# Performance work log

Measured on AMD Instinct MI355X. Metric: run time of the kernel, lower is better.

## Reference

```python
import jax, jax.numpy as jnp
import numpy as np

H_DIM = 256
N_HEADS = 8
HALF = H_DIM // 2

def _lin(x, W, b):
    # torch nn.Linear: y = x @ W.T + b
    y = x @ W.T
    return y + b if b is not None else y

def setup_inputs() -> dict:
    key = jax.random.key(0)
    ks = jax.random.split(key, 16)
    s = 0.02
    d = {
        'x': jax.random.normal(ks[0], (16, H_DIM, 32, 32), jnp.float32),
        'q1_w': jax.random.normal(ks[1], (HALF, HALF), jnp.float32) * s,
        'q1_b': jnp.zeros((HALF,), jnp.float32),
        'q2_w': jax.random.normal(ks[2], (HALF, HALF), jnp.float32) * s,
        'q2_b': jnp.zeros((HALF,), jnp.float32),
        'k1_w': jax.random.normal(ks[3], (HALF, HALF), jnp.float32) * s,
        'k1_b': jnp.zeros((HALF,), jnp.float32),
        'k2_w': jax.random.normal(ks[4], (HALF, HALF), jnp.float32) * s,
        'k2_b': jnp.zeros((HALF,), jnp.float32),
        'v1_w': jax.random.normal(ks[5], (HALF, HALF), jnp.float32) * s,
        'v1_b': jnp.zeros((HALF,), jnp.float32),
        'v2_w': jax.random.normal(ks[6], (HALF, HALF), jnp.float32) * s,
        'v2_b': jnp.zeros((HALF,), jnp.float32),
        'proj1_w': jax.random.normal(ks[7], (HALF, HALF), jnp.float32) * s,
        'proj1_b': jnp.zeros((HALF,), jnp.float32),
        'proj2_w': jax.random.normal(ks[8], (HALF, HALF), jnp.float32) * s,
        'proj2_b': jnp.zeros((HALF,), jnp.float32),
        'logit_scale': jnp.log(10.0 * jnp.ones((N_HEADS, 1, 1), jnp.float32)),
        'mlp_w1': jax.random.normal(ks[9], (128, 2), jnp.float32) * s,
        'mlp_b1': jnp.zeros((128,), jnp.float32),
        'mlp_w2': jax.random.normal(ks[10], (N_HEADS, 128), jnp.float32) * s,
    }
    return d

def _rel_pos_index(h, w):
    # static (numpy) relative position index, shape [N, N]
    ch, cw = np.meshgrid(np.arange(h), np.arange(w), indexing='ij')
    coords = np.stack([ch.reshape(-1), cw.reshape(-1)])  # [2, N]
    rel = coords[:, :, None] - coords[:, None, :]         # [2, N, N]
    rel = rel.transpose(1, 2, 0)
    rel[:, :, 0] += h - 1
    rel[:, :, 1] += w - 1
    return rel[:, :, 0] * (2 * w - 1) + rel[:, :, 1]

def _forward(x, q1_w, q1_b, q2_w, q2_b, k1_w, k1_b, k2_w, k2_b,
             v1_w, v1_b, v2_w, v2_b, proj1_w, proj1_b, proj2_w, proj2_b,
             logit_scale, mlp_w1, mlp_b1, mlp_w2):
    b, c, h, w = x.shape
    N = h * w
    nh = N_HEADS
    hd = c // nh
    x3 = jnp.transpose(x, (0, 2, 3, 1)).reshape(b, N, c)
    x0, x1 = x3[..., :c // 2], x3[..., c // 2:]

    def qkv(W0, b0, W1, b1):
        t = jnp.concatenate([x0 + _lin(x0, W0, b0), x1 + _lin(x1, W1, b1)], axis=-1)
        return t.reshape(b, N, nh, hd).transpose(0, 2, 1, 3)  # [b, nh, N, hd]

    q = qkv(q1_w, q1_b, q2_w, q2_b)
    k = qkv(k1_w, k1_b, k2_w, k2_b)
    v = qkv(v1_w, v1_b, v2_w, v2_b)

    eps = 1e-12
    qn = q / jnp.maximum(jnp.linalg.norm(q, axis=-1, keepdims=True), eps)
    kn = k / jnp.maximum(jnp.linalg.norm(k, axis=-1, keepdims=True), eps)
    attn = jnp.einsum('bhnd,bhmd->bhnm', qn, kn)  # cosine similarity
    scale = jnp.exp(jnp.minimum(logit_scale, jnp.log(1.0 / 0.01)))  # [nh,1,1]
    attn = attn * scale[None]

    # continuous relative-position bias (CPB) table via small MLP
    rch = jnp.arange(-(h - 1), h, dtype=jnp.float32) / (h - 1 + 1e-8)
    rcw = jnp.arange(-(w - 1), w, dtype=jnp.float32) / (w - 1 + 1e-8)
    gh, gw = jnp.meshgrid(rch, rcw, indexing='ij')
    tab = jnp.stack([gh, gw], axis=-1) * 3.2               # [2h-1, 2w-1, 2]
    tab = jnp.sign(tab) * (1.0 - jnp.exp(-jnp.abs(tab)))
    tab = jax.nn.relu(_lin(tab, mlp_w1, mlp_b1))
    tab = _lin(tab, mlp_w2, None).reshape(-1, nh)          # [(2h-1)(2w-1), nh]

    idx = jnp.asarray(_rel_pos_index(h, w))                # [N, N]
    bias = tab[idx.reshape(-1)].reshape(N, N, nh).transpose(2, 0, 1)
    bias = 16.0 * jax.nn.sigmoid(bias)
    attn = attn + bias[None]

    attn = jax.nn.softmax(attn, axis=-1)
    out = jnp.einsum('bhnm,bhmd->bhnd', attn, v).transpose(0, 2, 1, 3).reshape(b, N, c)
    o0, o1 = out[..., :c // 2], out[..., c // 2:]
    out = jnp.concatenate([_lin(o0, proj1_w, proj1_b), _lin(o1, proj2_w, proj2_b)], axis=-1)
    return out.reshape(b, h, w, c).transpose(0, 3, 1, 2)

def reference(x, q1_w, q1_b, q2_w, q2_b, k1_w, k1_b, k2_w, k2_b,
              v1_w, v1_b, v2_w, v2_b, proj1_w, proj1_b, proj2_w, proj2_b,
              logit_scale, mlp_w1, mlp_b1, mlp_w2):
    return _forward(x, q1_w, q1_b, q2_w, q2_b, k1_w, k1_b, k2_w, k2_b,
                    v1_w, v1_b, v2_w, v2_b, proj1_w, proj1_b, proj2_w, proj2_b,
                    logit_scale, mlp_w1, mlp_b1, mlp_w2)
```

## Files before the change

kernel.cpp:

```cpp
#include <hip/hip_runtime.h>
#include <cmath>


typedef _Float16 half_t;
typedef __attribute__((ext_vector_type(2))) __fp16 fp16x2;
typedef __attribute__((ext_vector_type(4))) _Float16 half4;
typedef __attribute__((ext_vector_type(8))) _Float16 half8;
typedef __attribute__((ext_vector_type(2))) float float2v;
typedef __attribute__((ext_vector_type(4))) float float4v;
typedef __attribute__((ext_vector_type(4))) unsigned int uint4v;

static __device__ __forceinline__ float4v mfma16(half8 a, half8 b, float4v c) {
  return __builtin_amdgcn_mfma_f32_16x16x32_f16(a, b, c, 0, 0, 0);
}

struct PtrArr8 { const float* p[8]; };

__global__ __launch_bounds__(256) void prep_w(PtrArr8 wsrc, PtrArr8 bsrc,
                                              half_t* __restrict__ wf,
                                              float* __restrict__ bws) {
  int y = blockIdx.y;
  const float* src = nullptr;
  const float* bs = nullptr;
#pragma unroll
  for (int i = 0; i < 8; i++)
    if (i == y) { src = wsrc.p[i]; bs = bsrc.p[i]; }
  int flat = (blockIdx.x * 256 + threadIdx.x) * 4;
  float4 w = *(const float4*)(src + flat);
  int j = flat >> 7, k = flat & 127;
  if (y < 6) {
    if (k == j)     w.x += 1.0f;
    if (k + 1 == j) w.y += 1.0f;
    if (k + 2 == j) w.z += 1.0f;
    if (k + 3 == j) w.w += 1.0f;
  }
  half4 h;
  h[0] = (half_t)w.x;
  h[1] = (half_t)w.y;
  h[2] = (half_t)w.z;
  h[3] = (half_t)w.w;
  int ng = j >> 4, l = j & 15, ks = k >> 5, quad = (k >> 3) & 3, o8 = k & 7;
  *(half4*)(wf + y * 16384 + ((ng * 4 + ks) * 64 + quad * 16 + l) * 8 + o8) =
      h;
  if (blockIdx.x == 0 && threadIdx.x < 128)
    bws[y * 128 + threadIdx.x] = bs[threadIdx.x];
}

__global__ __launch_bounds__(256) void bias_mlp(const float* __restrict__ w1,
                                                const float* __restrict__ b1,
                                                const float* __restrict__ w2,
                                                const float* __restrict__ ls,
                                                float* __restrict__ tabh2) {
  __shared__ float sw1[256];
  __shared__ float sb1[128];
  __shared__ float sw2[1024];
  int t = threadIdx.x;
  sw1[t] = w1[t];
  if (t < 128) sb1[t] = b1[t];
  for (int i = t; i < 1024; i += 256) sw2[i] = w2[i];
  __syncthreads();
  int p = blockIdx.x * 256 + t;
  if (p >= 3969) return;
  int ph = p / 63, pw = p % 63;
  float t0 = (float)(ph - 31) * (3.2f / 31.0f);
  float t1 = (float)(pw - 31) * (3.2f / 31.0f);
  t0 = copysignf(1.0f - __expf(-fabsf(t0)), t0);
  t1 = copysignf(1.0f - __expf(-fabsf(t1)), t1);
  float acc[8];
#pragma unroll
  for (int hh = 0; hh < 8; hh++) acc[hh] = 0.0f;
  for (int j = 0; j < 128; j++) {
    float hj = fmaxf(0.0f, t0 * sw1[2 * j] + t1 * sw1[2 * j + 1] + sb1[j]);
#pragma unroll
    for (int hh = 0; hh < 8; hh++) acc[hh] += hj * sw2[hh * 128 + j];
  }
  const float L2E = 1.44269504f;
#pragma unroll
  for (int hh = 0; hh < 8; hh++) {
    float scale = __expf(fminf(ls[hh], 4.6051702f));
    float c14 = 14.0f - (scale + 16.0f) * L2E;
    float bias = 16.0f / (1.0f + __expf(-acc[hh]));
    tabh2[hh * 3969 + p] = bias * L2E + c14;
  }
}

__global__ __launch_bounds__(256, 4) void qkv_mfma(
    const float* __restrict__ x, const half_t* __restrict__ wfrag,
    const float* __restrict__ lscale, const float* __restrict__ bws,
    half_t* __restrict__ qf, half_t* __restrict__ kf,
    half_t* __restrict__ vf) {
  __shared__ half_t tbuf[4608];
  int t = threadIdx.x;
  int lane = t & 63, wv = t >> 6, l = lane & 15, quad = lane >> 4;
  int rw = wv & 1, cw = wv >> 1;
  int hf = blockIdx.y;
  int m0 = blockIdx.x * 32;
  int b = m0 >> 10, n0 = m0 & 1023;

  half8 afr[4];
  {
    const float* xb =
        x + ((size_t)b * 256 + hf * 128) * 1024 + n0 + rw * 16 + l;
#pragma unroll
    for (int ks = 0; ks < 4; ks++) {
      half8 a;
#pragma unroll
      for (int j = 0; j < 8; j++)
        a[j] = (half_t)xb[(size_t)(ks * 32 + quad * 8 + j) * 1024];
      afr[ks] = a;
    }
  }

  for (int op = 0; op < 3; op++) {
    int combo = op * 2 + hf;
    const half_t* wfb = wfrag + combo * 16384;
    float4v acc[4];
#pragma unroll
    for (int ngl = 0; ngl < 4; ngl++) {
      int ng = cw * 4 + ngl;
      float4v c = {0.f, 0.f, 0.f, 0.f};
#pragma unroll
      for (int ks = 0; ks < 4; ks++) {
        half8 bfrag =
            *(const half8*)(wfb + ((ng * 4 + ks) * 64 + lane) * 8);
        c = mfma16(afr[ks], bfrag, c);
      }
      acc[ngl] = c;
    }
#pragma unroll
    for (int ngl = 0; ngl < 4; ngl++) {
      float bb = bws[combo * 128 + (cw * 4 + ngl) * 16 + l];
#pragma unroll
      for (int r2 = 0; r2 < 4; r2++) acc[ngl][r2] += bb;
    }
    if (op < 2) {
#pragma unroll
      for (int hgl = 0; hgl < 2; hgl++) {
        float sc = 1.0f;
        if (op == 0)
          sc = __expf(fminf(lscale[hf * 4 + cw * 2 + hgl], 4.6051702f)) *
               1.44269504f;
#pragma unroll
        for (int r2 = 0; r2 < 4; r2++) {
          float ss = acc[2 * hgl][r2] * acc[2 * hgl][r2] +
                     acc[2 * hgl + 1][r2] * acc[2 * hgl + 1][r2];
          ss += __shfl_xor(ss, 1, 64);
          ss += __shfl_xor(ss, 2, 64);
          ss += __shfl_xor(ss, 4, 64);
          ss += __shfl_xor(ss, 8, 64);
          float rn = sc / fmaxf(sqrtf(ss), 1e-12f);
          acc[2 * hgl][r2] *= rn;
          acc[2 * hgl + 1][r2] *= rn;
        }
      }
#pragma unroll
      for (int ngl = 0; ngl < 4; ngl++)
#pragma unroll
        for (int r2 = 0; r2 < 4; r2++)
          tbuf[(rw * 16 + quad * 4 + r2) * 136 + (cw * 4 + ngl) * 16 + l] =
              (half_t)acc[ngl][r2];
      __syncthreads();
      half_t* dst = (op == 0) ? qf : kf;
#pragma unroll
      for (int i = 0; i < 2; i++) {
        int idx = t + 256 * i;
        int row = idx >> 4, colc = (idx & 15) * 8;
        half8 vv = *(const half8*)(tbuf + row * 136 + colc);
        int head = hf * 4 + (colc >> 5), d = colc & 31;
        *(half8*)(dst + (((size_t)b * 8 + head) * 1024 + n0 + row) * 32 + d) =
            vv;
      }
      __syncthreads();
    } else {
#pragma unroll
      for (int ngl = 0; ngl < 4; ngl++) {
        int col = (cw * 4 + ngl) * 16 + l;
        half4 hv;
#pragma unroll
        for (int r2 = 0; r2 < 4; r2++) hv[r2] = (half_t)acc[ngl][r2];
        *(half4*)(tbuf + col * 36 + rw * 16 + quad * 4) = hv;
      }
      __syncthreads();
      int p64 = (n0 >> 5) & 1;
      int nb64 = n0 & ~63;
#pragma unroll
      for (int i = 0; i < 8; i++) {
        int idx = t + 256 * i;
        int col = idx >> 4, rp = idx & 15;
        unsigned int val = *(const unsigned int*)(tbuf + col * 36 + rp * 2);
        int head = hf * 4 + (col >> 5);
        int d = col & 31;
        int npos = nb64 + ((rp >> 1) & 3) * 16 + (rp & 1) * 8 + p64 * 4 +
                   ((rp >> 3) & 1) * 2;
        *(unsigned int*)((char*)vf +
                         (((((size_t)b * 8 + head) * 32 + d) * 1024) + npos) *
                             2) = val;
      }
    }
  }
}


#define LOADK(kt)                                                           \
  {                                                                         \
    _Pragma("unroll") for (int nt = 0; nt < 4; nt++)                        \
        kfr[nt] = *(const half8*)(kbase + ((kt)*64 + nt * 16 + l) * 32 +    \
                                  quad * 8);                                \
  }

#define LOADV(kt)                                                           \
  {                                                                         \
    _Pragma("unroll") for (int ks = 0; ks < 2; ks++) {                      \
      vv0[ks] = *(const half8*)(vbase + l * 1024 + (kt)*64 + quad * 16 +    \
                                ks * 8);                                    \
      vv1[ks] = *(const half8*)(vbase + (16 + l) * 1024 + (kt)*64 +         \
                                quad * 16 + ks * 8);                        \
    }                                                                       \
  }

#define QK_PHASE(kt, S, SR)                                                 \
  {                                                                         \
    int rowb = (wv + 31 - 2 * (kt)) * 63 + cA + (S)*16;                     \
    _Pragma("unroll") for (int nt = 0; nt < 4; nt++) {                      \
      int base = rowb - (nt >> 1) * 63 - (nt & 1) * 16;                     \
      float2v p0 = sb2d[base];                                              \
      float2v p1 = sb2d[base - 2];                                          \
      float4v c;                                                            \
      c[0] = p0[1];                                                         \
      c[1] = p0[0];                                                         \
      c[2] = p1[1];                                                         \
      c[3] = p1[0];                                                         \
      SR[nt] = mfma16(kfr[nt], qfr[S], c);                                  \
    }                                                                       \
  }

#define EXP_PACK(S, SR)                                                     \
  {                                                                         \
    unsigned int w0[4], w1[4];                                              \
    _Pragma("unroll") for (int nt = 0; nt < 4; nt++) {                      \
      fp16x2 plo = __builtin_amdgcn_cvt_pkrtz(exp2f(SR[nt][0]),             \
                                              exp2f(SR[nt][1]));            \
      fp16x2 phi = __builtin_amdgcn_cvt_pkrtz(exp2f(SR[nt][2]),             \
                                              exp2f(SR[nt][3]));            \
      w0[nt] = __builtin_bit_cast(unsigned int, plo);                       \
      w1[nt] = __builtin_bit_cast(unsigned int, phi);                       \
    }                                                                       \
    uint4v u0 = {w0[0], w0[1], w0[2], w0[3]};                               \
    uint4v u1 = {w1[0], w1[1], w1[2], w1[3]};                               \
    pf##S[0] = __builtin_bit_cast(half8, u0);                               \
    pf##S[1] = __builtin_bit_cast(half8, u1);                               \
  }

#define PV_PHASE(S)                                                         \
  {                                                                         \
    _Pragma("unroll") for (int ks = 0; ks < 2; ks++) {                      \
      o0[S] = mfma16(pf##S[ks], vv0[ks], o0[S]);                            \
      o1[S] = mfma16(pf##S[ks], vv1[ks], o1[S]);                            \
      accl[S] = mfma16(pf##S[ks], ones, accl[S]);                           \
    }                                                                       \
  }

__global__ __launch_bounds__(256) void attn_mfma(
    const half_t* __restrict__ qf, const half_t* __restrict__ kf,
    const half_t* __restrict__ vf, const float* __restrict__ tabh2,
    half_t* __restrict__ ao) {
  __shared__ float2v sb2d[2205];

  int id = blockIdx.x;
  int qo = id >> 7;
  int bh = id & 127;
  int h = bh & 7, b = bh >> 3;
  int t = threadIdx.x;
  int lane = t & 63, wv = t >> 6, l = lane & 15, quad = lane >> 4;
  size_t bhs = (size_t)b * 8 + h;
  const half_t* kbase = kf + bhs * 1024 * 32;
  const half_t* vbase = vf + bhs * 32 * 1024;
  int row0 = qo * 128 + wv * 32;
  int cA = l + 31 - quad * 4;

  half8 kfr[4], vv0[2], vv1[2], qfr[2], pf0[2], pf1[2];
  LOADK(0);
  LOADV(0);
#pragma unroll
  for (int s = 0; s < 2; s++)
    qfr[s] = *(const half8*)(qf + (bhs * 1024 + row0 + s * 16 + l) * 32 +
                             quad * 8);

  {
    const float* tb = tabh2 + h * 3969 + qo * 252;
    for (int i = t; i < 2205; i += 256) {
      float2v pr;
      pr[0] = (i > 0) ? tb[i - 1] : 0.0f;
      pr[1] = tb[i];
      sb2d[i] = pr;
    }
  }

  float4v o0[2], o1[2], accl[2];
#pragma unroll
  for (int s = 0; s < 2; s++) {
    o0[s] = (float4v){0.f, 0.f, 0.f, 0.f};
    o1[s] = (float4v){0.f, 0.f, 0.f, 0.f};
    accl[s] = (float4v){0.f, 0.f, 0.f, 0.f};
  }
  half8 ones;
#pragma unroll
  for (int j = 0; j < 8; j++) ones[j] = (half_t)1.0f;

  __syncthreads();

#pragma unroll
  for (int kt = 0; kt < 16; ++kt) {
    float4v sres[4];
    QK_PHASE(kt, 0, sres);
    EXP_PACK(0, sres);
    float4v sres2[4];
    QK_PHASE(kt, 1, sres2);
    if (kt < 15) LOADK(kt + 1);
    EXP_PACK(1, sres2);
    PV_PHASE(0);
    PV_PHASE(1);
    if (kt < 15) LOADV(kt + 1);
  }

#pragma unroll
  for (int s = 0; s < 2; s++) {
#pragma unroll
    for (int r2 = 0; r2 < 4; r2++) {
      float linv = 1.0f / accl[s][r2];
      size_t rowaddr =
          ((size_t)b * 1024 + row0 + s * 16 + quad * 4 + r2) * 256 + h * 32;
      ao[rowaddr + l] = (half_t)(o0[s][r2] * linv);
      ao[rowaddr + 16 + l] = (half_t)(o1[s][r2] * linv);
    }
  }
}

__global__ __launch_bounds__(256, 4) void proj_mfma(
    const half_t* __restrict__ ao, const half_t* __restrict__ wfrag,
    const float* __restrict__ bws, float* __restrict__ out) {
  __shared__ float yt[128 * 36];
  int t = threadIdx.x;
  int lane = t & 63, wv = t >> 6, l = lane & 15, quad = lane >> 4;
  int rw = wv & 1, cw = wv >> 1;
  int hf = blockIdx.y;
  int m0 = blockIdx.x * 32;
  int b = m0 >> 10, n0 = m0 & 1023;

  half8 afr[4];
  const half_t* ab =
      ao + ((size_t)m0 + rw * 16 + l) * 256 + hf * 128 + quad * 8;
#pragma unroll
  for (int ks = 0; ks < 4; ks++) afr[ks] = *(const half8*)(ab + ks * 32);

  const half_t* wfb = wfrag + (6 + hf) * 16384;
#pragma unroll
  for (int ngl = 0; ngl < 4; ngl++) {
    int ng = cw * 4 + ngl;
    float4v c = {0.f, 0.f, 0.f, 0.f};
#pragma unroll
    for (int ks = 0; ks < 4; ks++) {
      half8 bfrag = *(const half8*)(wfb + ((ng * 4 + ks) * 64 + lane) * 8);
      c = mfma16(afr[ks], bfrag, c);
    }
    float bb = bws[(6 + hf) * 128 + ng * 16 + l];
#pragma unroll
    for (int r2 = 0; r2 < 4; r2++) c[r2] += bb;
    *(float4v*)(yt + (ng * 16 + l) * 36 + rw * 16 + quad * 4) = c;
  }
  __syncthreads();
#pragma unroll
  for (int i = 0; i < 4; i++) {
    int idx = t + 256 * i;
    int col = idx >> 3, rg = idx & 7;
    float4v vv = *(const float4v*)(yt + col * 36 + rg * 4);
    *(float4v*)(out + ((size_t)b * 256 + hf * 128 + col) * 1024 + n0 +
                rg * 4) = vv;
  }
}

extern "C" void kernel_launch(void* const* d_in, const int* in_sizes, int n_in,
                              void* d_out, int out_size, void* d_ws,
                              size_t ws_size, hipStream_t stream) {
  (void)in_sizes; (void)n_in; (void)out_size; (void)ws_size;
  const float* x = (const float*)d_in[0];

  half_t* ws = (half_t*)d_ws;
  half_t* qfp = ws;
  half_t* kfp = ws + 4194304;
  half_t* vfp = ws + 8388608;
  half_t* aop = ws + 12582912;
  half_t* wfp = ws + 16777216;
  float* tabh2 = (float*)((char*)d_ws + 33816576);
  float* bws = (float*)((char*)d_ws + 33943584);

  PtrArr8 wsrc, bsrc;
  const int widx[8] = {1, 3, 5, 7, 9, 11, 13, 15};
  for (int i = 0; i < 8; i++) {
    wsrc.p[i] = (const float*)d_in[widx[i]];
    bsrc.p[i] = (const float*)d_in[widx[i] + 1];
  }

  prep_w<<<dim3(16, 8), 256, 0, stream>>>(wsrc, bsrc, wfp, bws);
  bias_mlp<<<16, 256, 0, stream>>>((const float*)d_in[18],
                                   (const float*)d_in[19],
                                   (const float*)d_in[20],
                                   (const float*)d_in[17], tabh2);
  qkv_mfma<<<dim3(512, 2), 256, 0, stream>>>(x, wfp, (const float*)d_in[17],
                                             bws, qfp, kfp, vfp);
  attn_mfma<<<1024, 256, 0, stream>>>(qfp, kfp, vfp, tabh2, aop);
  proj_mfma<<<dim3(512, 2), 256, 0, stream>>>(aop, wfp, bws, (float*)d_out);
}
```

Baseline: 190.9 us.

## Merge prep kernels, store bias as float4 quads, use raw exp2 intrinsic

Merges the weight-prep and bias-MLP kernels into one launch, which saves a kernel launch and its serialization. In the attention kernel, the shared-memory bias table now holds four shifted floats per entry, so each MFMA accumulator init is one float4 LDS read instead of two float2 reads and a shuffle. The shared table doubles in size, which may lower occupancy. Calls to exp2f are replaced by the hardware exp2 builtin to avoid range-handling overhead.

```diff
diff --git a/kernel.cpp b/kernel.cpp
--- a/kernel.cpp
+++ b/kernel.cpp
@@ -6,7 +6,6 @@
 typedef __attribute__((ext_vector_type(2))) __fp16 fp16x2;
 typedef __attribute__((ext_vector_type(4))) _Float16 half4;
 typedef __attribute__((ext_vector_type(8))) _Float16 half8;
-typedef __attribute__((ext_vector_type(2))) float float2v;
 typedef __attribute__((ext_vector_type(4))) float float4v;
 typedef __attribute__((ext_vector_type(4))) unsigned int uint4v;
 
@@ -16,71 +15,70 @@
 
 struct PtrArr8 { const float* p[8]; };
 
-__global__ __launch_bounds__(256) void prep_w(PtrArr8 wsrc, PtrArr8 bsrc,
-                                              half_t* __restrict__ wf,
-                                              float* __restrict__ bws) {
-  int y = blockIdx.y;
-  const float* src = nullptr;
-  const float* bs = nullptr;
-#pragma unroll
-  for (int i = 0; i < 8; i++)
-    if (i == y) { src = wsrc.p[i]; bs = bsrc.p[i]; }
-  int flat = (blockIdx.x * 256 + threadIdx.x) * 4;
-  float4 w = *(const float4*)(src + flat);
-  int j = flat >> 7, k = flat & 127;
-  if (y < 6) {
-    if (k == j)     w.x += 1.0f;
-    if (k + 1 == j) w.y += 1.0f;
-    if (k + 2 == j) w.z += 1.0f;
-    if (k + 3 == j) w.w += 1.0f;
-  }
-  half4 h;
-  h[0] = (half_t)w.x;
-  h[1] = (half_t)w.y;
-  h[2] = (half_t)w.z;
-  h[3] = (half_t)w.w;
-  int ng = j >> 4, l = j & 15, ks = k >> 5, quad = (k >> 3) & 3, o8 = k & 7;
-  *(half4*)(wf + y * 16384 + ((ng * 4 + ks) * 64 + quad * 16 + l) * 8 + o8) =
-      h;
-  if (blockIdx.x == 0 && threadIdx.x < 128)
-    bws[y * 128 + threadIdx.x] = bs[threadIdx.x];
-}
-
-__global__ __launch_bounds__(256) void bias_mlp(const float* __restrict__ w1,
-                                                const float* __restrict__ b1,
-                                                const float* __restrict__ w2,
-                                                const float* __restrict__ ls,
-                                                float* __restrict__ tabh2) {
-  __shared__ float sw1[256];
-  __shared__ float sb1[128];
-  __shared__ float sw2[1024];
+__global__ __launch_bounds__(256) void prep_all(
+    PtrArr8 wsrc, PtrArr8 bsrc, half_t* __restrict__ wf,
+    float* __restrict__ bws, const float* __restrict__ w1,
+    const float* __restrict__ b1, const float* __restrict__ w2,
+    const float* __restrict__ ls, float* __restrict__ tabh2) {
+  __shared__ float smem[1408];
+  int blk = blockIdx.x;
   int t = threadIdx.x;
-  sw1[t] = w1[t];
-  if (t < 128) sb1[t] = b1[t];
-  for (int i = t; i < 1024; i += 256) sw2[i] = w2[i];
-  __syncthreads();
-  int p = blockIdx.x * 256 + t;
-  if (p >= 3969) return;
-  int ph = p / 63, pw = p % 63;
-  float t0 = (float)(ph - 31) * (3.2f / 31.0f);
-  float t1 = (float)(pw - 31) * (3.2f / 31.0f);
-  t0 = copysignf(1.0f - __expf(-fabsf(t0)), t0);
-  t1 = copysignf(1.0f - __expf(-fabsf(t1)), t1);
-  float acc[8];
-#pragma unroll
-  for (int hh = 0; hh < 8; hh++) acc[hh] = 0.0f;
-  for (int j = 0; j < 128; j++) {
-    float hj = fmaxf(0.0f, t0 * sw1[2 * j] + t1 * sw1[2 * j + 1] + sb1[j]);
-#pragma unroll
-    for (int hh = 0; hh < 8; hh++) acc[hh] += hj * sw2[hh * 128 + j];
-  }
-  const float L2E = 1.44269504f;
-#pragma unroll
-  for (int hh = 0; hh < 8; hh++) {
-    float scale = __expf(fminf(ls[hh], 4.6051702f));
-    float c14 = 14.0f - (scale + 16.0f) * L2E;
-    float bias = 16.0f / (1.0f + __expf(-acc[hh]));
-    tabh2[hh * 3969 + p] = bias * L2E + c14;
+  if (blk < 128) {
+    int y = blk >> 4, xx = blk & 15;
+    const float* src = nullptr;
+    const float* bs = nullptr;
+#pragma unroll
+    for (int i = 0; i < 8; i++)
+      if (i == y) { src = wsrc.p[i]; bs = bsrc.p[i]; }
+    int flat = (xx * 256 + t) * 4;
+    float4 w = *(const float4*)(src + flat);
+    int j = flat >> 7, k = flat & 127;
+    if (y < 6) {
+      if (k == j)     w.x += 1.0f;
+      if (k + 1 == j) w.y += 1.0f;
+      if (k + 2 == j) w.z += 1.0f;
+      if (k + 3 == j) w.w += 1.0f;
+    }
+    half4 h;
+    h[0] = (half_t)w.x;
+    h[1] = (half_t)w.y;
+    h[2] = (half_t)w.z;
+    h[3] = (half_t)w.w;
+    int ng = j >> 4, l = j & 15, ks = k >> 5, quad = (k >> 3) & 3, o8 = k & 7;
+    *(half4*)(wf + y * 16384 + ((ng * 4 + ks) * 64 + quad * 16 + l) * 8 +
+              o8) = h;
+    if (xx == 0 && t < 128) bws[y * 128 + t] = bs[t];
+  } else {
+    float* sw1 = smem;
+    float* sb1 = smem + 256;
+    float* sw2 = smem + 384;
+    sw1[t] = w1[t];
+    if (t < 128) sb1[t] = b1[t];
+    for (int i = t; i < 1024; i += 256) sw2[i] = w2[i];
+    __syncthreads();
+    int p = (blk - 128) * 256 + t;
+    if (p >= 3969) return;
+    int ph = p / 63, pw = p % 63;
+    float t0 = (float)(ph - 31) * (3.2f / 31.0f);
+    float t1 = (float)(pw - 31) * (3.2f / 31.0f);
+    t0 = copysignf(1.0f - __expf(-fabsf(t0)), t0);
+    t1 = copysignf(1.0f - __expf(-fabsf(t1)), t1);
+    float acc[8];
+#pragma unroll
+    for (int hh = 0; hh < 8; hh++) acc[hh] = 0.0f;
+    for (int j = 0; j < 128; j++) {
+      float hj = fmaxf(0.0f, t0 * sw1[2 * j] + t1 * sw1[2 * j + 1] + sb1[j]);
+#pragma unroll
+      for (int hh = 0; hh < 8; hh++) acc[hh] += hj * sw2[hh * 128 + j];
+    }
+    const float L2E = 1.44269504f;
+#pragma unroll
+    for (int hh = 0; hh < 8; hh++) {
+      float scale = __expf(fminf(ls[hh], 4.6051702f));
+      float c14 = 14.0f - (scale + 16.0f) * L2E;
+      float bias = 16.0f / (1.0f + __expf(-acc[hh]));
+      tabh2[hh * 3969 + p] = bias * L2E + c14;
+    }
   }
 }
 
@@ -223,14 +221,7 @@
     int rowb = (wv + 31 - 2 * (kt)) * 63 + cA + (S)*16;                     \
     _Pragma("unroll") for (int nt = 0; nt < 4; nt++) {                      \
       int base = rowb - (nt >> 1) * 63 - (nt & 1) * 16;                     \
-      float2v p0 = sb2d[base];                                              \
-      float2v p1 = sb2d[base - 2];                                          \
-      float4v c;                                                            \
-      c[0] = p0[1];                                                         \
-      c[1] = p0[0];                                                         \
-      c[2] = p1[1];                                                         \
-      c[3] = p1[0];                                                         \
-      SR[nt] = mfma16(kfr[nt], qfr[S], c);                                  \
+      SR[nt] = mfma16(kfr[nt], qfr[S], sb2q[base]);                         \
     }                                                                       \
   }
 
@@ -238,10 +229,12 @@
   {                                                                         \
     unsigned int w0[4], w1[4];                                              \
     _Pragma("unroll") for (int nt = 0; nt < 4; nt++) {                      \
-      fp16x2 plo = __builtin_amdgcn_cvt_pkrtz(exp2f(SR[nt][0]),             \
-                                              exp2f(SR[nt][1]));            \
-      fp16x2 phi = __builtin_amdgcn_cvt_pkrtz(exp2f(SR[nt][2]),             \
-                                              exp2f(SR[nt][3]));            \
+      fp16x2 plo = __builtin_amdgcn_cvt_pkrtz(                              \
+          __builtin_amdgcn_exp2f(SR[nt][0]),                                \
+          __builtin_amdgcn_exp2f(SR[nt][1]));                               \
+      fp16x2 phi = __builtin_amdgcn_cvt_pkrtz(                              \
+          __builtin_amdgcn_exp2f(SR[nt][2]),                                \
+          __builtin_amdgcn_exp2f(SR[nt][3]));                               \
       w0[nt] = __builtin_bit_cast(unsigned int, plo);                       \
       w1[nt] = __builtin_bit_cast(unsigned int, phi);                       \
     }                                                                       \
@@ -264,7 +257,7 @@
     const half_t* __restrict__ qf, const half_t* __restrict__ kf,
     const half_t* __restrict__ vf, const float* __restrict__ tabh2,
     half_t* __restrict__ ao) {
-  __shared__ float2v sb2d[2205];
+  __shared__ float4v sb2q[2205];
 
   int id = blockIdx.x;
   int qo = id >> 7;
@@ -289,10 +282,12 @@
   {
     const float* tb = tabh2 + h * 3969 + qo * 252;
     for (int i = t; i < 2205; i += 256) {
-      float2v pr;
-      pr[0] = (i > 0) ? tb[i - 1] : 0.0f;
-      pr[1] = tb[i];
-      sb2d[i] = pr;
+      float4v pr;
+      pr[0] = tb[i];
+      pr[1] = (i > 0) ? tb[i - 1] : 0.0f;
+      pr[2] = (i > 1) ? tb[i - 2] : 0.0f;
+      pr[3] = (i > 2) ? tb[i - 3] : 0.0f;
+      sb2q[i] = pr;
     }
   }
 
@@ -401,11 +396,11 @@
     bsrc.p[i] = (const float*)d_in[widx[i] + 1];
   }
 
-  prep_w<<<dim3(16, 8), 256, 0, stream>>>(wsrc, bsrc, wfp, bws);
-  bias_mlp<<<16, 256, 0, stream>>>((const float*)d_in[18],
-                                   (const float*)d_in[19],
-                                   (const float*)d_in[20],
-                                   (const float*)d_in[17], tabh2);
+  prep_all<<<144, 256, 0, stream>>>(wsrc, bsrc, wfp, bws,
+                                    (const float*)d_in[18],
+                                    (const float*)d_in[19],
+                                    (const float*)d_in[20],
+                                    (const float*)d_in[17], tabh2);
   qkv_mfma<<<dim3(512, 2), 256, 0, stream>>>(x, wfp, (const float*)d_in[17],
                                              bws, qfp, kfp, vfp);
   attn_mfma<<<1024, 256, 0, stream>>>(qfp, kfp, vfp, tabh2, aop);
```

New measurement: 188.5 us. No clear change (-1.2%).
